# Performance work log

Hardware: AMD Instinct MI355X
Metric: run time of the kernel (lower is better)

## Reference

```python
import jax, jax.numpy as jnp
import numpy as np

T, B = 100, 256
DIMS = [784, 1024, 256]
DT, TAU_M, TAU_S = 1e-3, 0.02, 0.005
ALPHA = 1.0 - DT / TAU_S   # 0.8  (synaptic current decay)
BETA = 1.0 - DT / TAU_M    # 0.95 (membrane decay)


def lif_forward(x, W):
    """EventProp LIF layer forward. x: [T,B,d1], W: [d2,d1].
    Matches SpikingLinear_ev.manual_forward: step i uses input[i-1]; step 0 is all zeros.
    Returns spikes [T,B,d2], pre-reset voltage V_spikes, current I."""
    Bsz, d2 = x.shape[1], W.shape[0]
    I0 = jnp.zeros((Bsz, d2), x.dtype)
    V0 = jnp.zeros((Bsz, d2), x.dtype)

    def step(carry, x_t):
        I_prev, V_prev = carry
        I = ALPHA * I_prev + x_t @ W.T
        V_pre = BETA * V_prev + (1.0 - BETA) * I
        s = (V_pre > 1.0).astype(x.dtype)
        V = (1.0 - s) * V_pre  # reset-to-zero on spike
        return (I, V), (s, V_pre, I)

    _, (s, V_pre, I) = jax.lax.scan(step, (I0, V0), x[:-1])
    pad = jnp.zeros((1, Bsz, d2), x.dtype)
    spikes = jnp.concatenate([pad, s], axis=0)
    V_spikes = jnp.concatenate([pad, V_pre], axis=0)
    I_full = jnp.concatenate([pad, I], axis=0)
    return spikes, V_spikes, I_full


def setup_inputs() -> dict:
    key = jax.random.key(0)
    k1, k2, k3 = jax.random.split(key, 3)
    x = (jax.random.uniform(k1, (T, B, DIMS[0])) < 0.05).astype(jnp.float32)
    # kaiming_normal_ on [d2,d1]: std = sqrt(2/fan_in), fan_in = d1
    W1 = jax.random.normal(k2, (DIMS[1], DIMS[0]), jnp.float32) * np.float32(np.sqrt(2.0 / DIMS[0]))
    W2 = jax.random.normal(k3, (DIMS[2], DIMS[1]), jnp.float32) * np.float32(np.sqrt(2.0 / DIMS[1]))
    return {"x": x, "W1": W1, "W2": W2}


def reference(x, W1, W2):
    s1, _, _ = lif_forward(x, W1)
    s2, _, _ = lif_forward(s1, W2)
    return s2
```

## Files before the change

kernel.cpp:

```cpp
#include <hip/hip_runtime.h>
#include <hip/hip_bf16.h>


#define ALPHA_F 0.8f
#define BETA_F 0.95f
#define ONE_MINUS_BETA_F 0.05f

typedef float f4_nt __attribute__((ext_vector_type(4)));

__global__ __launch_bounds__(256) void prep(const float* __restrict__ x,
                                            const float* __restrict__ W1,
                                            const float* __restrict__ W2,
                                            float* __restrict__ W1T,
                                            float* __restrict__ W2T,
                                            int* __restrict__ cnts,
                                            int* __restrict__ lists) {
    __shared__ float tile[32][33];
    const int bid = blockIdx.x;
    const int tid = threadIdx.x;

    if (bid < 6272) {
        const int r = bid * 4 + (tid >> 6);
        const int lane = tid & 63;
        const int k0 = lane * 4;
        unsigned flags = 0;
        if (lane < 49) {
            float4 v = *(const float4*)(x + (size_t)r * 784 + k0);
            flags = (v.x != 0.0f ? 1u : 0u) | (v.y != 0.0f ? 2u : 0u) |
                    (v.z != 0.0f ? 4u : 0u) | (v.w != 0.0f ? 8u : 0u);
        }
        const unsigned long long m0 = __ballot(flags & 1u);
        const unsigned long long m1 = __ballot(flags & 2u);
        const unsigned long long m2 = __ballot(flags & 4u);
        const unsigned long long m3 = __ballot(flags & 8u);
        const int c0 = __popcll(m0), c1 = __popcll(m1), c2 = __popcll(m2);
        const unsigned long long lm = ((unsigned long long)1 << lane) - 1;
        int* lrow = lists + (size_t)r * 160;
        if (flags & 1u) lrow[__popcll(m0 & lm)] = k0 + 0;
        if (flags & 2u) lrow[c0 + __popcll(m1 & lm)] = k0 + 1;
        if (flags & 4u) lrow[c0 + c1 + __popcll(m2 & lm)] = k0 + 2;
        if (flags & 8u) lrow[c0 + c1 + c2 + __popcll(m3 & lm)] = k0 + 3;
        if (lane == 0) cnts[r] = c0 + c1 + c2 + __popcll(m3);
    } else {
        const float* W; float* WT; int N, K, tk, tn;
        if (bid < 7072) {
            W = W1; WT = W1T; N = 1024; K = 784;
            const int i = bid - 6272; tk = i % 25; tn = i / 25;
        } else {
            W = W2; WT = W2T; N = 256; K = 1024;
            const int i = bid - 7072; tk = i % 32; tn = i / 32;
        }
        const int k0 = tk * 32, n0 = tn * 32;
        const int tx = tid & 31, ty = tid >> 5;
#pragma unroll
        for (int r = 0; r < 4; ++r) {
            int n = n0 + ty + r * 8, k = k0 + tx;
            if (n < N && k < K) tile[ty + r * 8][tx] = W[(size_t)n * K + k];
        }
        __syncthreads();
#pragma unroll
        for (int r = 0; r < 4; ++r) {
            int k = k0 + ty + r * 8, n = n0 + tx;
            if (k < K && n < N) WT[(size_t)k * N + n] = tile[tx][ty + r * 8];
        }
    }
}

__global__ __launch_bounds__(256) void sparse1(const int* __restrict__ cnts,
                                               const int* __restrict__ lists,
                                               const float* __restrict__ W1T,
                                               float* __restrict__ C1) {
    const int tid = threadIdx.x;
    const int row = blockIdx.x;
    const int n = cnts[row];
    const int* lst = lists + (size_t)row * 160;
    const float* wbase = W1T + tid * 4;
    float4 acc = {0.0f, 0.0f, 0.0f, 0.0f};
    int i = 0;
    for (; i + 8 <= n; i += 8) {
        float4 w0 = *(const float4*)(wbase + (size_t)lst[i + 0] * 1024);
        float4 w1 = *(const float4*)(wbase + (size_t)lst[i + 1] * 1024);
        float4 w2 = *(const float4*)(wbase + (size_t)lst[i + 2] * 1024);
        float4 w3 = *(const float4*)(wbase + (size_t)lst[i + 3] * 1024);
        float4 w4 = *(const float4*)(wbase + (size_t)lst[i + 4] * 1024);
        float4 w5 = *(const float4*)(wbase + (size_t)lst[i + 5] * 1024);
        float4 w6 = *(const float4*)(wbase + (size_t)lst[i + 6] * 1024);
        float4 w7 = *(const float4*)(wbase + (size_t)lst[i + 7] * 1024);
        acc.x += ((w0.x + w1.x) + (w2.x + w3.x)) + ((w4.x + w5.x) + (w6.x + w7.x));
        acc.y += ((w0.y + w1.y) + (w2.y + w3.y)) + ((w4.y + w5.y) + (w6.y + w7.y));
        acc.z += ((w0.z + w1.z) + (w2.z + w3.z)) + ((w4.z + w5.z) + (w6.z + w7.z));
        acc.w += ((w0.w + w1.w) + (w2.w + w3.w)) + ((w4.w + w5.w) + (w6.w + w7.w));
    }
    for (; i < n; ++i) {
        float4 w0 = *(const float4*)(wbase + (size_t)lst[i] * 1024);
        acc.x += w0.x; acc.y += w0.y; acc.z += w0.z; acc.w += w0.w;
    }
    f4_nt o = {acc.x, acc.y, acc.z, acc.w};
    __builtin_nontemporal_store(o, (f4_nt*)(C1 + (size_t)row * 1024 + tid * 4));
}

__global__ __launch_bounds__(256) void scan1(const float* __restrict__ C1,
                                             unsigned long long* __restrict__ S1b) {
    const int idx = blockIdx.x * 256 + threadIdx.x;
    const int word = idx >> 6;
    const int lane = threadIdx.x & 63;
    if (lane == 0) S1b[word] = 0ull;
    float I = 0.0f, V = 0.0f;
#pragma unroll 7
    for (int t = 1; t <= 98; ++t) {
        float c = C1[(size_t)(t - 1) * 262144 + idx];
        I = ALPHA_F * I + c;
        float Vp = BETA_F * V + ONE_MINUS_BETA_F * I;
        const bool sp = Vp > 1.0f;
        unsigned long long m = __ballot(sp);
        V = sp ? 0.0f : Vp;
        if (lane == 0) S1b[(size_t)t * 4096 + word] = m;
    }
}

__global__ __launch_bounds__(256) void sparse2(const unsigned long long* __restrict__ S1b,
                                               const float* __restrict__ W2T,
                                               float* __restrict__ C2) {
    const int r = __builtin_amdgcn_readfirstlane(blockIdx.x * 4 + (threadIdx.x >> 6));
    const int lane = threadIdx.x & 63;
    const unsigned long long* mrow = S1b + (size_t)r * 16;
    float4 acc = {0, 0, 0, 0};
#pragma unroll 1
    for (int j = 0; j < 16; ++j) {
        unsigned long long m = mrow[j];
        while (m) {
            const int bit = __ffsll((long long)m) - 1;
            m &= m - 1;
            const int k = j * 64 + bit;
            float4 w = *(const float4*)(W2T + (size_t)k * 256 + lane * 4);
            acc.x += w.x; acc.y += w.y; acc.z += w.z; acc.w += w.w;
        }
    }
    *(float4*)(C2 + (size_t)r * 256 + lane * 4) = acc;
}

__global__ __launch_bounds__(256) void scan2(const float* __restrict__ C2,
                                             float* __restrict__ out) {
    const int idx = blockIdx.x * 256 + threadIdx.x;
    __builtin_nontemporal_store(0.0f, out + idx);
    float I = 0.0f, V = 0.0f;
#pragma unroll 9
    for (int t = 1; t <= 99; ++t) {
        float c = C2[(size_t)(t - 1) * 65536 + idx];
        I = ALPHA_F * I + c;
        float Vp = BETA_F * V + ONE_MINUS_BETA_F * I;
        float s = (Vp > 1.0f) ? 1.0f : 0.0f;
        V = (1.0f - s) * Vp;
        __builtin_nontemporal_store(s, out + (size_t)t * 65536 + idx);
    }
}

extern "C" void kernel_launch(void* const* d_in, const int* in_sizes, int n_in,
                              void* d_out, int out_size, void* d_ws, size_t ws_size,
                              hipStream_t stream) {
    const float* x  = (const float*)d_in[0];
    const float* W1 = (const float*)d_in[1];
    const float* W2 = (const float*)d_in[2];
    float* out = (float*)d_out;

    char* ws = (char*)d_ws;
    float* C1 = (float*)ws;
    unsigned long long* S1b = (unsigned long long*)(ws + 102760448);
    float* W1T = (float*)(ws + 106004480);
    float* W2T = (float*)(ws + 109215744);
    int* cnts  = (int*)(ws + 110264320);
    int* lists = (int*)(ws + 110364672);
    float* C2 = C1;

    prep<<<7328, 256, 0, stream>>>(x, W1, W2, W1T, W2T, cnts, lists);
    sparse1<<<25088, 256, 0, stream>>>(cnts, lists, W1T, C1);
    scan1<<<1024, 256, 0, stream>>>(C1, S1b);
    sparse2<<<25344 / 4, 256, 0, stream>>>(S1b, W2T, C2);
    scan2<<<256, 256, 0, stream>>>(C2, out);
}
```

Measured before the change: 248.6 us.

## Fuse layer-2 sparse gather with its LIF scan and batch scan1 loads

```diff
diff --git a/kernel.cpp b/kernel.cpp
--- a/kernel.cpp
+++ b/kernel.cpp
@@ -106,52 +106,54 @@
     const int lane = threadIdx.x & 63;
     if (lane == 0) S1b[word] = 0ull;
     float I = 0.0f, V = 0.0f;
-#pragma unroll 7
-    for (int t = 1; t <= 98; ++t) {
-        float c = C1[(size_t)(t - 1) * 262144 + idx];
-        I = ALPHA_F * I + c;
-        float Vp = BETA_F * V + ONE_MINUS_BETA_F * I;
-        const bool sp = Vp > 1.0f;
-        unsigned long long m = __ballot(sp);
-        V = sp ? 0.0f : Vp;
-        if (lane == 0) S1b[(size_t)t * 4096 + word] = m;
+    for (int t0 = 1; t0 <= 85; t0 += 14) {
+        float c[14];
+#pragma unroll
+        for (int j = 0; j < 14; ++j)
+            c[j] = C1[(size_t)(t0 - 1 + j) * 262144 + idx];
+#pragma unroll
+        for (int j = 0; j < 14; ++j) {
+            I = ALPHA_F * I + c[j];
+            float Vp = BETA_F * V + ONE_MINUS_BETA_F * I;
+            const bool sp = Vp > 1.0f;
+            unsigned long long m = __ballot(sp);
+            V = sp ? 0.0f : Vp;
+            if (lane == 0) S1b[(size_t)(t0 + j) * 4096 + word] = m;
+        }
     }
 }
 
-__global__ __launch_bounds__(256) void sparse2(const unsigned long long* __restrict__ S1b,
-                                               const float* __restrict__ W2T,
-                                               float* __restrict__ C2) {
-    const int r = __builtin_amdgcn_readfirstlane(blockIdx.x * 4 + (threadIdx.x >> 6));
-    const int lane = threadIdx.x & 63;
-    const unsigned long long* mrow = S1b + (size_t)r * 16;
-    float4 acc = {0, 0, 0, 0};
+__global__ __launch_bounds__(256) void layer2(const unsigned long long* __restrict__ S1b,
+                                              const float* __restrict__ W2T,
+                                              float* __restrict__ out) {
+    __shared__ unsigned long long masks[99 * 16];
+    const int b = blockIdx.x;
+    const int tid = threadIdx.x;
+    for (int i = tid; i < 99 * 16; i += 256) {
+        const int tt = i >> 4, j = i & 15;
+        masks[i] = S1b[(size_t)tt * 4096 + b * 16 + j];
+    }
+    __syncthreads();
+
+    __builtin_nontemporal_store(0.0f, out + b * 256 + tid);
+    float I = 0.0f, V = 0.0f;
+    for (int t = 1; t <= 99; ++t) {
+        const unsigned long long* mrow = &masks[(t - 1) * 16];
+        float c = 0.0f;
 #pragma unroll 1
-    for (int j = 0; j < 16; ++j) {
-        unsigned long long m = mrow[j];
-        while (m) {
-            const int bit = __ffsll((long long)m) - 1;
-            m &= m - 1;
-            const int k = j * 64 + bit;
-            float4 w = *(const float4*)(W2T + (size_t)k * 256 + lane * 4);
-            acc.x += w.x; acc.y += w.y; acc.z += w.z; acc.w += w.w;
+        for (int j = 0; j < 16; ++j) {
+            unsigned long long m = mrow[j];
+            while (m) {
+                const int bit = __ffsll((long long)m) - 1;
+                m &= m - 1;
+                c += W2T[(size_t)(j * 64 + bit) * 256 + tid];
+            }
         }
-    }
-    *(float4*)(C2 + (size_t)r * 256 + lane * 4) = acc;
-}
-
-__global__ __launch_bounds__(256) void scan2(const float* __restrict__ C2,
-                                             float* __restrict__ out) {
-    const int idx = blockIdx.x * 256 + threadIdx.x;
-    __builtin_nontemporal_store(0.0f, out + idx);
-    float I = 0.0f, V = 0.0f;
-#pragma unroll 9
-    for (int t = 1; t <= 99; ++t) {
-        float c = C2[(size_t)(t - 1) * 65536 + idx];
         I = ALPHA_F * I + c;
         float Vp = BETA_F * V + ONE_MINUS_BETA_F * I;
         float s = (Vp > 1.0f) ? 1.0f : 0.0f;
         V = (1.0f - s) * Vp;
-        __builtin_nontemporal_store(s, out + (size_t)t * 65536 + idx);
+        __builtin_nontemporal_store(s, out + (size_t)t * 65536 + b * 256 + tid);
     }
 }
 
@@ -170,11 +172,9 @@
     float* W2T = (float*)(ws + 109215744);
     int* cnts  = (int*)(ws + 110264320);
     int* lists = (int*)(ws + 110364672);
-    float* C2 = C1;
 
     prep<<<7328, 256, 0, stream>>>(x, W1, W2, W1T, W2T, cnts, lists);
     sparse1<<<25088, 256, 0, stream>>>(cnts, lists, W1T, C1);
     scan1<<<1024, 256, 0, stream>>>(C1, S1b);
-    sparse2<<<25344 / 4, 256, 0, stream>>>(S1b, W2T, C2);
-    scan2<<<256, 256, 0, stream>>>(C2, out);
+    layer2<<<256, 256, 0, stream>>>(S1b, W2T, out);
 }
```

Result: slower. 296.7 us (+19.3%).
